# Optimization experiments

Hardware: AMD Instinct MI355X
Metric: run time of the kernel (lower is better)

The kernel has to match this reference:

```python
import jax, jax.numpy as jnp
import numpy as np

NUM_EXPERTS = 64
TOP_K = 2
CAPACITY_FACTOR = 1.25
D_MODEL = 2048
BATCH, SEQ = 4, 4096


def setup_inputs() -> dict:
    key = jax.random.key(0)
    kx, kw = jax.random.split(key)
    x = jax.random.normal(kx, (BATCH, SEQ, D_MODEL), dtype=jnp.float32)
    # router weight: Linear(input_dim, num_experts, bias=False), init std=0.001
    W = jax.random.normal(kw, (NUM_EXPERTS, D_MODEL), dtype=jnp.float32) * 0.001
    return {"x": x, "W": W}


def reference(x, W):
    B, S, D = x.shape
    N = B * S  # combined batch of tokens
    E = NUM_EXPERTS
    k = TOP_K
    capacity = int(CAPACITY_FACTOR * N * k / E)  # static Python int

    x_flat = x.reshape(N, D)
    router_logits = jnp.einsum('nd,ed->ne', x_flat, W)  # [N, E]
    routing_weights = jax.nn.softmax(router_logits, axis=-1)

    top_k_weights, top_k_indices = jax.lax.top_k(routing_weights, k)  # [N, k]
    top_k_weights = top_k_weights / (top_k_weights.sum(-1, keepdims=True) + 1e-8)

    expert_counts = jnp.zeros((E,), dtype=jnp.float32)
    dispatch_mask = jnp.zeros((N, E), dtype=jnp.float32)
    token_ids = jnp.arange(N)

    # Sequential over k (fixed, small): within a k-step the capacity check uses
    # counts from previous steps only, matching the torch scatter semantics.
    for k_idx in range(k):
        expert_idx = top_k_indices[:, k_idx]            # [N]
        under_cap = expert_counts[expert_idx] < capacity  # [N] bool
        expert_counts = expert_counts + jax.ops.segment_sum(
            under_cap.astype(jnp.float32), expert_idx, num_segments=E)
        # top-k experts are distinct per token, so add == set on zero-init slots
        dispatch_mask = dispatch_mask.at[token_ids, expert_idx].add(
            jnp.where(under_cap, top_k_weights[:, k_idx], 0.0))

    # Tokens that got dropped everywhere go to the least-loaded expert with w=1
    unrouted = dispatch_mask.sum(-1) == 0                     # [N]
    least_loaded = jnp.argmax(capacity - expert_counts)       # scalar
    dispatch_mask = jnp.where(
        unrouted[:, None] & (jnp.arange(E)[None, :] == least_loaded),
        1.0, dispatch_mask)

    normalized_dispatch_mask = dispatch_mask / (dispatch_mask.sum(-1, keepdims=True) + 1e-8)

    router_z_loss = jnp.mean(jnp.square(router_logits))
    counts = normalized_dispatch_mask.sum(0)                  # [E]
    target_count = float(N * k / E)
    load_balance_loss = jnp.mean(jnp.square(counts / float(N) - target_count / float(N)))
    router_loss = 0.001 * jax.lax.stop_gradient(router_z_loss) \
                + 0.001 * jax.lax.stop_gradient(load_balance_loss)

    return (jax.lax.stop_gradient(routing_weights), normalized_dispatch_mask, router_loss)
```

## Files before the change

kernel.cpp:

```cpp
#include <hip/hip_runtime.h>
#include <math.h>

#define N_TOK 16384
#define D_MODEL 2048
#define N_EXP 64
#define CAPACITY 640
#define NREP 8

#define BK 64
#define NSTAGE (D_MODEL / BK)
#define LPW 72

typedef __attribute__((ext_vector_type(8))) _Float16 h8;
typedef __attribute__((ext_vector_type(4))) float f4;

__global__ __launch_bounds__(256, 1) void k12_gemm_softmax(
    const float* __restrict__ x, const float* __restrict__ W,
    float* __restrict__ rw_out, int2* __restrict__ top12,
    float2* __restrict__ wts, int* __restrict__ histR,
    float* __restrict__ zR) {
  __shared__ __align__(16) _Float16 WHs[2][64][LPW];
  __shared__ __align__(16) _Float16 WLs[2][64][LPW];
  __shared__ float slog[64][65];
  __shared__ float zred[4];

  const int t = threadIdx.x;
  const int lane = t & 63;
  const int wid = t >> 6;
  const int m0 = blockIdx.x * 64;
  const int rep = blockIdx.x & (NREP - 1);

  const int we = t >> 2;
  const int wc = (t & 3) * 16;
  const int frow = lane & 15;
  const int fk = (lane >> 4) * 8;

  const float* wg = W + (size_t)we * D_MODEL + wc;
  const float* xg = x + (size_t)(m0 + wid * 16 + frow) * D_MODEL + fk;

  float4 wreg[2][4], xreg[2][4];
  h8 afh[2][2], afl[2][2];
  f4 acc1[4], acc2[4];
#pragma unroll
  for (int i = 0; i < 4; i++) {
    acc1[i] = (f4)(0.f);
    acc2[i] = (f4)(0.f);
  }

#define LOAD_W(slot, s)                        \
  {                                            \
    const float* p_ = wg + (s) * BK;           \
    wreg[slot][0] = *(const float4*)(p_);      \
    wreg[slot][1] = *(const float4*)(p_ + 4);  \
    wreg[slot][2] = *(const float4*)(p_ + 8);  \
    wreg[slot][3] = *(const float4*)(p_ + 12); \
  }
#define LOAD_X(slot, s)                        \
  {                                            \
    const float* p_ = xg + (s) * BK;           \
    xreg[slot][0] = *(const float4*)(p_);      \
    xreg[slot][1] = *(const float4*)(p_ + 4);  \
    xreg[slot][2] = *(const float4*)(p_ + 32); \
    xreg[slot][3] = *(const float4*)(p_ + 36); \
  }

#define CVTSTORE_W(slot, buf)                                           \
  {                                                                     \
    float wf[16] = {wreg[slot][0].x, wreg[slot][0].y, wreg[slot][0].z,  \
                    wreg[slot][0].w, wreg[slot][1].x, wreg[slot][1].y,  \
                    wreg[slot][1].z, wreg[slot][1].w, wreg[slot][2].x,  \
                    wreg[slot][2].y, wreg[slot][2].z, wreg[slot][2].w,  \
                    wreg[slot][3].x, wreg[slot][3].y, wreg[slot][3].z,  \
                    wreg[slot][3].w};                                   \
    h8 h0, h1, l0, l1;                                                  \
    _Pragma("unroll") for (int j = 0; j < 8; j++) {                     \
      float s0 = wf[j] * 1024.f;                                        \
      _Float16 a_ = (_Float16)s0;                                       \
      h0[j] = a_;                                                       \
      l0[j] = (_Float16)((s0 - (float)a_) * 1024.f);                    \
      float s1 = wf[j + 8] * 1024.f;                                    \
      _Float16 b_ = (_Float16)s1;                                       \
      h1[j] = b_;                                                       \
      l1[j] = (_Float16)((s1 - (float)b_) * 1024.f);                    \
    }                                                                   \
    *(h8*)&WHs[buf][we][wc] = h0;                                       \
    *(h8*)&WHs[buf][we][wc + 8] = h1;                                   \
    *(h8*)&WLs[buf][we][wc] = l0;                                       \
    *(h8*)&WLs[buf][we][wc + 8] = l1;                                   \
  }

#define CVT_X(slot)                                                    \
  {                                                                    \
    float xf[16] = {xreg[slot][0].x, xreg[slot][0].y, xreg[slot][0].z, \
                    xreg[slot][0].w, xreg[slot][1].x, xreg[slot][1].y, \
                    xreg[slot][1].z, xreg[slot][1].w, xreg[slot][2].x, \
                    xreg[slot][2].y, xreg[slot][2].z, xreg[slot][2].w, \
                    xreg[slot][3].x, xreg[slot][3].y, xreg[slot][3].z, \
                    xreg[slot][3].w};                                  \
    _Pragma("unroll") for (int j = 0; j < 8; j++) {                    \
      _Float16 a_ = (_Float16)xf[j];                                   \
      afh[slot][0][j] = a_;                                            \
      afl[slot][0][j] = (_Float16)((xf[j] - (float)a_) * 1024.f);      \
      _Float16 b_ = (_Float16)xf[j + 8];                               \
      afh[slot][1][j] = b_;                                            \
      afl[slot][1][j] = (_Float16)((xf[j + 8] - (float)b_) * 1024.f);  \
    }                                                                  \
  }

#define COMPUTE(buf, p)                                                      \
  {                                                                          \
    _Pragma("unroll") for (int ks = 0; ks < 2; ks++) {                       \
      _Pragma("unroll") for (int nt = 0; nt < 4; nt++) {                     \
        h8 bh = *(const h8*)&WHs[buf][nt * 16 + frow][ks * 32 + fk];         \
        h8 bl = *(const h8*)&WLs[buf][nt * 16 + frow][ks * 32 + fk];         \
        acc1[nt] = __builtin_amdgcn_mfma_f32_16x16x32_f16(afh[p][ks], bh,    \
                                                          acc1[nt], 0, 0, 0); \
        acc2[nt] = __builtin_amdgcn_mfma_f32_16x16x32_f16(afl[p][ks], bh,    \
                                                          acc2[nt], 0, 0, 0); \
        acc2[nt] = __builtin_amdgcn_mfma_f32_16x16x32_f16(afh[p][ks], bl,    \
                                                          acc2[nt], 0, 0, 0); \
      }                                                                      \
    }                                                                        \
  }

#define PHASE(p, s)                 \
  {                                 \
    if ((s) + 1 < NSTAGE) {         \
      CVTSTORE_W(1 - (p), 1 - (p)); \
      CVT_X(1 - (p));               \
    }                               \
    if ((s) + 3 < NSTAGE) {         \
      LOAD_W(1 - (p), (s) + 3);     \
      LOAD_X(1 - (p), (s) + 3);     \
    }                               \
    COMPUTE((p), (p));              \
    __syncthreads();                \
  }

  LOAD_W(0, 0);
  LOAD_X(0, 0);
  LOAD_W(1, 1);
  LOAD_X(1, 1);
  CVTSTORE_W(0, 0);
  CVT_X(0);
  LOAD_W(0, 2);
  LOAD_X(0, 2);
  __syncthreads();

  for (int it = 0; it < NSTAGE; it += 2) {
    PHASE(0, it);
    PHASE(1, it + 1);
  }

  const int cg = lane >> 4, ci = lane & 15;
#pragma unroll
  for (int nt = 0; nt < 4; nt++)
#pragma unroll
    for (int r = 0; r < 4; r++) {
      const float v =
          (acc1[nt][r] + acc2[nt][r] * 0.0009765625f) * 0.0009765625f;
      slog[wid * 16 + cg * 4 + r][nt * 16 + ci] = v;
    }

  float z_acc = 0.f;
  for (int tt = 0; tt < 16; tt++) {
    const int tloc = wid * 16 + tt;
    const int n = m0 + tloc;
    const float v = slog[tloc][lane];
    z_acc += v * v;
    float mx = v;
#pragma unroll
    for (int off = 32; off; off >>= 1) mx = fmaxf(mx, __shfl_xor(mx, off));
    const float p = __expf(v - mx);
    float ssum = p;
#pragma unroll
    for (int off = 32; off; off >>= 1) ssum += __shfl_xor(ssum, off);
    const float rw = p / ssum;
    rw_out[(size_t)n * N_EXP + lane] = rw;

    const unsigned long long b1 = __ballot(v == mx);
    const int i1 = __builtin_ctzll(b1);
    float v2 = (lane == i1) ? -INFINITY : v;
#pragma unroll
    for (int off = 32; off; off >>= 1) v2 = fmaxf(v2, __shfl_xor(v2, off));
    const unsigned long long b2 = __ballot(v == v2) & ~(1ull << i1);
    const int i2 = __builtin_ctzll(b2);
    const float rw1 = __shfl(rw, i1);
    const float rw2 = __shfl(rw, i2);
    if (lane == 0) {
      const float denom = rw1 + rw2 + 1e-8f;
      top12[n] = make_int2(i1, i2);
      wts[n] = make_float2(rw1 / denom, rw2 / denom);
      atomicAdd(&histR[(rep * N_EXP + i1) * 16], 1);
    }
  }
#pragma unroll
  for (int off = 32; off; off >>= 1) z_acc += __shfl_xor(z_acc, off);
  if (lane == 0) zred[wid] = z_acc;
  __syncthreads();
  if (t == 0) atomicAdd(&zR[rep * 16], zred[0] + zred[1] + zred[2] + zred[3]);
}

__global__ __launch_bounds__(256) void k3_dispatch(
    const int2* __restrict__ top12, const float2* __restrict__ wts,
    const int* __restrict__ histR, float* __restrict__ mask_out,
    float* __restrict__ cntR) {
  const int lane = threadIdx.x & 63;
  const int wid = threadIdx.x >> 6;
  const int n = blockIdx.x * 4 + wid;
  const int rep = blockIdx.x & (NREP - 1);

  const int2 ij = top12[n];
  const float2 w = wts[n];
  int h = 0;
#pragma unroll
  for (int r = 0; r < NREP; r++) h += histR[(r * N_EXP + ij.y) * 16];
  const bool allowed = h < CAPACITY;
  const float ssum = w.x + (allowed ? w.y : 0.f);
  const float inv = 1.f / (ssum + 1e-8f);
  float val = 0.f;
  if (lane == ij.x) val = w.x * inv;
  else if (allowed && lane == ij.y) val = w.y * inv;
  mask_out[(size_t)n * N_EXP + lane] = val;
  if (val != 0.f) atomicAdd(&cntR[(rep * N_EXP + lane) * 16], val);
}

__global__ void k4_loss(const float* __restrict__ cntR,
                        const float* __restrict__ zR,
                        float* __restrict__ loss_out) {
  const int lane = threadIdx.x;
  float c = 0.f;
#pragma unroll
  for (int r = 0; r < NREP; r++) c += cntR[(r * N_EXP + lane) * 16];
  const float d = (c - 512.0f) * (1.0f / 16384.0f);
  float v = d * d;
#pragma unroll
  for (int off = 32; off; off >>= 1) v += __shfl_xor(v, off);
  if (lane == 0) {
    float z = 0.f;
#pragma unroll
    for (int r = 0; r < NREP; r++) z += zR[r * 16];
    const float lb = v * (1.0f / 64.0f);
    loss_out[0] = 0.001f * (z * (1.0f / (16384.0f * 64.0f))) + 0.001f * lb;
  }
}

extern "C" void kernel_launch(void* const* d_in, const int* in_sizes, int n_in,
                              void* d_out, int out_size, void* d_ws,
                              size_t ws_size, hipStream_t stream) {
  const float* x = (const float*)d_in[0];
  const float* W = (const float*)d_in[1];
  float* out = (float*)d_out;
  float* rw_out = out;
  float* mask_out = out + (size_t)N_TOK * N_EXP;
  float* loss_out = out + 2 * (size_t)N_TOK * N_EXP;

  char* ws = (char*)d_ws;
  int* histR = (int*)ws;
  float* cntR = (float*)(ws + 32768);
  float* zR = (float*)(ws + 65536);
  int2* top12 = (int2*)(ws + 131072);
  float2* wts = (float2*)(ws + 262144);

  hipMemsetAsync(histR, 0, 65536 + 512, stream);
  k12_gemm_softmax<<<256, 256, 0, stream>>>(x, W, rw_out, top12, wts, histR,
                                            zR);
  k3_dispatch<<<N_TOK / 4, 256, 0, stream>>>(top12, wts, histR, mask_out,
                                             cntR);
  k4_loss<<<1, 64, 0, stream>>>(cntR, zR, loss_out);
}
```

Baseline: 228.5 us.

## Pre-split router weights into fp16 hi/lo once and halve GEMM row tile

Adds a small prologue kernel that converts W into fp16 high/low halves in workspace once, so the GEMM kernel loads ready fp16 data instead of reconverting W in every block. The GEMM block tile drops from 64 to 32 tokens, with the four waves arranged 2x2 over tokens and experts. This doubles the grid to 512 blocks and allows two blocks per CU, which targets low occupancy on a 256-CU part. The cost is an extra kernel launch and twice as many blocks each streaming the full W, plus an extra barrier before the softmax epilogue.

```diff
diff --git a/kernel.cpp b/kernel.cpp
--- a/kernel.cpp
+++ b/kernel.cpp
@@ -14,46 +14,70 @@
 typedef __attribute__((ext_vector_type(8))) _Float16 h8;
 typedef __attribute__((ext_vector_type(4))) float f4;
 
-__global__ __launch_bounds__(256, 1) void k12_gemm_softmax(
-    const float* __restrict__ x, const float* __restrict__ W,
-    float* __restrict__ rw_out, int2* __restrict__ top12,
-    float2* __restrict__ wts, int* __restrict__ histR,
-    float* __restrict__ zR) {
+__global__ __launch_bounds__(256) void k0_cvtw(const float* __restrict__ W,
+                                               _Float16* __restrict__ WHg,
+                                               _Float16* __restrict__ WLg) {
+  const int i = (blockIdx.x * 256 + threadIdx.x) * 8;
+  const float4 a = *(const float4*)(W + i);
+  const float4 b = *(const float4*)(W + i + 4);
+  const float f[8] = {a.x, a.y, a.z, a.w, b.x, b.y, b.z, b.w};
+  h8 hh, ll;
+#pragma unroll
+  for (int j = 0; j < 8; j++) {
+    const float s = f[j] * 1024.f;
+    const _Float16 h = (_Float16)s;
+    hh[j] = h;
+    ll[j] = (_Float16)((s - (float)h) * 1024.f);
+  }
+  *(h8*)(WHg + i) = hh;
+  *(h8*)(WLg + i) = ll;
+}
+
+__global__ __launch_bounds__(256, 2) void k12_gemm_softmax(
+    const float* __restrict__ x, const _Float16* __restrict__ WHg,
+    const _Float16* __restrict__ WLg, float* __restrict__ rw_out,
+    int2* __restrict__ top12, float2* __restrict__ wts,
+    int* __restrict__ histR, float* __restrict__ zR) {
   __shared__ __align__(16) _Float16 WHs[2][64][LPW];
   __shared__ __align__(16) _Float16 WLs[2][64][LPW];
-  __shared__ float slog[64][65];
+  __shared__ float slog[32][65];
   __shared__ float zred[4];
 
   const int t = threadIdx.x;
   const int lane = t & 63;
   const int wid = t >> 6;
-  const int m0 = blockIdx.x * 64;
+  const int wm = wid >> 1;
+  const int wn = wid & 1;
+  const int m0 = blockIdx.x * 32;
   const int rep = blockIdx.x & (NREP - 1);
 
   const int we = t >> 2;
-  const int wc = (t & 3) * 16;
+  const int wcc = (t & 3) * 16;
   const int frow = lane & 15;
   const int fk = (lane >> 4) * 8;
 
-  const float* wg = W + (size_t)we * D_MODEL + wc;
-  const float* xg = x + (size_t)(m0 + wid * 16 + frow) * D_MODEL + fk;
-
-  float4 wreg[2][4], xreg[2][4];
+  const _Float16* whg = WHg + (size_t)we * D_MODEL + wcc;
+  const _Float16* wlg = WLg + (size_t)we * D_MODEL + wcc;
+  const float* xg = x + (size_t)(m0 + wm * 16 + frow) * D_MODEL + fk;
+
+  h8 wh[2][2], wl[2][2];
+  float4 xreg[2][4];
   h8 afh[2][2], afl[2][2];
-  f4 acc1[4], acc2[4];
-#pragma unroll
-  for (int i = 0; i < 4; i++) {
+  f4 acc1[2], acc2[2];
+#pragma unroll
+  for (int i = 0; i < 2; i++) {
     acc1[i] = (f4)(0.f);
     acc2[i] = (f4)(0.f);
   }
 
-#define LOAD_W(slot, s)                        \
-  {                                            \
-    const float* p_ = wg + (s) * BK;           \
-    wreg[slot][0] = *(const float4*)(p_);      \
-    wreg[slot][1] = *(const float4*)(p_ + 4);  \
-    wreg[slot][2] = *(const float4*)(p_ + 8);  \
-    wreg[slot][3] = *(const float4*)(p_ + 12); \
+#define LOAD_W(slot, s)                             \
+  {                                                 \
+    const _Float16* ph_ = whg + (s) * BK;           \
+    const _Float16* pl_ = wlg + (s) * BK;           \
+    wh[slot][0] = *(const h8*)(ph_);                \
+    wh[slot][1] = *(const h8*)(ph_ + 8);            \
+    wl[slot][0] = *(const h8*)(pl_);                \
+    wl[slot][1] = *(const h8*)(pl_ + 8);            \
   }
 #define LOAD_X(slot, s)                        \
   {                                            \
@@ -63,32 +87,13 @@
     xreg[slot][2] = *(const float4*)(p_ + 32); \
     xreg[slot][3] = *(const float4*)(p_ + 36); \
   }
-
-#define CVTSTORE_W(slot, buf)                                           \
-  {                                                                     \
-    float wf[16] = {wreg[slot][0].x, wreg[slot][0].y, wreg[slot][0].z,  \
-                    wreg[slot][0].w, wreg[slot][1].x, wreg[slot][1].y,  \
-                    wreg[slot][1].z, wreg[slot][1].w, wreg[slot][2].x,  \
-                    wreg[slot][2].y, wreg[slot][2].z, wreg[slot][2].w,  \
-                    wreg[slot][3].x, wreg[slot][3].y, wreg[slot][3].z,  \
-                    wreg[slot][3].w};                                   \
-    h8 h0, h1, l0, l1;                                                  \
-    _Pragma("unroll") for (int j = 0; j < 8; j++) {                     \
-      float s0 = wf[j] * 1024.f;                                        \
-      _Float16 a_ = (_Float16)s0;                                       \
-      h0[j] = a_;                                                       \
-      l0[j] = (_Float16)((s0 - (float)a_) * 1024.f);                    \
-      float s1 = wf[j + 8] * 1024.f;                                    \
-      _Float16 b_ = (_Float16)s1;                                       \
-      h1[j] = b_;                                                       \
-      l1[j] = (_Float16)((s1 - (float)b_) * 1024.f);                    \
-    }                                                                   \
-    *(h8*)&WHs[buf][we][wc] = h0;                                       \
-    *(h8*)&WHs[buf][we][wc + 8] = h1;                                   \
-    *(h8*)&WLs[buf][we][wc] = l0;                                       \
-    *(h8*)&WLs[buf][we][wc + 8] = l1;                                   \
-  }
-
+#define STORE_W(slot, buf)                     \
+  {                                            \
+    *(h8*)&WHs[buf][we][wcc] = wh[slot][0];    \
+    *(h8*)&WHs[buf][we][wcc + 8] = wh[slot][1]; \
+    *(h8*)&WLs[buf][we][wcc] = wl[slot][0];    \
+    *(h8*)&WLs[buf][we][wcc + 8] = wl[slot][1]; \
+  }
 #define CVT_X(slot)                                                    \
   {                                                                    \
     float xf[16] = {xreg[slot][0].x, xreg[slot][0].y, xreg[slot][0].z, \
@@ -106,27 +111,25 @@
       afl[slot][1][j] = (_Float16)((xf[j + 8] - (float)b_) * 1024.f);  \
     }                                                                  \
   }
-
-#define COMPUTE(buf, p)                                                      \
-  {                                                                          \
-    _Pragma("unroll") for (int ks = 0; ks < 2; ks++) {                       \
-      _Pragma("unroll") for (int nt = 0; nt < 4; nt++) {                     \
-        h8 bh = *(const h8*)&WHs[buf][nt * 16 + frow][ks * 32 + fk];         \
-        h8 bl = *(const h8*)&WLs[buf][nt * 16 + frow][ks * 32 + fk];         \
-        acc1[nt] = __builtin_amdgcn_mfma_f32_16x16x32_f16(afh[p][ks], bh,    \
-                                                          acc1[nt], 0, 0, 0); \
-        acc2[nt] = __builtin_amdgcn_mfma_f32_16x16x32_f16(afl[p][ks], bh,    \
-                                                          acc2[nt], 0, 0, 0); \
-        acc2[nt] = __builtin_amdgcn_mfma_f32_16x16x32_f16(afh[p][ks], bl,    \
-                                                          acc2[nt], 0, 0, 0); \
-      }                                                                      \
-    }                                                                        \
-  }
-
+#define COMPUTE(buf, p)                                                       \
+  {                                                                           \
+    _Pragma("unroll") for (int ks = 0; ks < 2; ks++) {                        \
+      _Pragma("unroll") for (int nt = 0; nt < 2; nt++) {                      \
+        h8 bh = *(const h8*)&WHs[buf][wn * 32 + nt * 16 + frow][ks * 32 + fk]; \
+        h8 bl = *(const h8*)&WLs[buf][wn * 32 + nt * 16 + frow][ks * 32 + fk]; \
+        acc1[nt] = __builtin_amdgcn_mfma_f32_16x16x32_f16(afh[p][ks], bh,     \
+                                                          acc1[nt], 0, 0, 0);  \
+        acc2[nt] = __builtin_amdgcn_mfma_f32_16x16x32_f16(afl[p][ks], bh,     \
+                                                          acc2[nt], 0, 0, 0);  \
+        acc2[nt] = __builtin_amdgcn_mfma_f32_16x16x32_f16(afh[p][ks], bl,     \
+                                                          acc2[nt], 0, 0, 0);  \
+      }                                                                       \
+    }                                                                         \
+  }
 #define PHASE(p, s)                 \
   {                                 \
     if ((s) + 1 < NSTAGE) {         \
-      CVTSTORE_W(1 - (p), 1 - (p)); \
+      STORE_W(1 - (p), 1 - (p));    \
       CVT_X(1 - (p));               \
     }                               \
     if ((s) + 3 < NSTAGE) {         \
@@ -141,7 +144,7 @@
   LOAD_X(0, 0);
   LOAD_W(1, 1);
   LOAD_X(1, 1);
-  CVTSTORE_W(0, 0);
+  STORE_W(0, 0);
   CVT_X(0);
   LOAD_W(0, 2);
   LOAD_X(0, 2);
@@ -154,17 +157,18 @@
 
   const int cg = lane >> 4, ci = lane & 15;
 #pragma unroll
-  for (int nt = 0; nt < 4; nt++)
+  for (int nt = 0; nt < 2; nt++)
 #pragma unroll
     for (int r = 0; r < 4; r++) {
       const float v =
           (acc1[nt][r] + acc2[nt][r] * 0.0009765625f) * 0.0009765625f;
-      slog[wid * 16 + cg * 4 + r][nt * 16 + ci] = v;
+      slog[wm * 16 + cg * 4 + r][wn * 32 + nt * 16 + ci] = v;
     }
+  __syncthreads();
 
   float z_acc = 0.f;
-  for (int tt = 0; tt < 16; tt++) {
-    const int tloc = wid * 16 + tt;
+  for (int tt = 0; tt < 8; tt++) {
+    const int tloc = wid * 8 + tt;
     const int n = m0 + tloc;
     const float v = slog[tloc][lane];
     z_acc += v * v;
@@ -261,10 +265,13 @@
   float* zR = (float*)(ws + 65536);
   int2* top12 = (int2*)(ws + 131072);
   float2* wts = (float2*)(ws + 262144);
+  _Float16* WHg = (_Float16*)(ws + 393216);
+  _Float16* WLg = (_Float16*)(ws + 655360);
 
   hipMemsetAsync(histR, 0, 65536 + 512, stream);
-  k12_gemm_softmax<<<256, 256, 0, stream>>>(x, W, rw_out, top12, wts, histR,
-                                            zR);
+  k0_cvtw<<<64, 256, 0, stream>>>(W, WHg, WLg);
+  k12_gemm_softmax<<<512, 256, 0, stream>>>(x, WHg, WLg, rw_out, top12, wts,
+                                            histR, zR);
   k3_dispatch<<<N_TOK / 4, 256, 0, stream>>>(top12, wts, histR, mask_out,
                                              cntR);
   k4_loss<<<1, 64, 0, stream>>>(cntR, zR, loss_out);
```

After: 222.5 us. 2.6% less time.
